# Kernel optimization log

Measured on AMD Instinct MI355X. Metric: run time of the kernel, lower is better.

Reference implementation:

```python
import jax, jax.numpy as jnp
import numpy as np

T, N, E, F_IN, H1, H2, NUM_GRAPHS, K = 8, 10000, 320000, 32, 32, 16, 64, 5


def setup_inputs() -> dict:
    key = jax.random.key(0)
    ks = jax.random.split(key, 16)
    p = lambda k, shape: jax.random.normal(k, shape, jnp.float32) * 0.05
    return {
        "x": jax.random.normal(ks[0], (T, N, F_IN), jnp.float32),
        "edge_index": jax.random.randint(ks[1], (2, E), 0, N),
        "edge_attr": jax.random.uniform(ks[2], (E,), jnp.float32),
        "batch": jnp.sort(jax.random.randint(ks[3], (N,), 0, NUM_GRAPHS)),
        "Wx1": p(ks[4], (4, K, F_IN, H1)),
        "bx1": jnp.zeros((4, H1), jnp.float32),
        "Wh1": p(ks[5], (4, K, H1, H1)),
        "bh1": jnp.zeros((4, H1), jnp.float32),
        "wc1": p(ks[6], (3, H1)),
        "b1": jnp.zeros((4, H1), jnp.float32),
        "Wx2": p(ks[7], (4, K, H1, H2)),
        "bx2": jnp.zeros((4, H2), jnp.float32),
        "Wh2": p(ks[8], (4, K, H2, H2)),
        "bh2": jnp.zeros((4, H2), jnp.float32),
        "wc2": p(ks[9], (3, H2)),
        "b2": jnp.zeros((4, H2), jnp.float32),
        "lin_w": p(ks[10], (H2, 1)),
        "lin_b": jnp.zeros((1,), jnp.float32),
    }


def _forward(x, edge_index, edge_attr, batch,
             Wx1, bx1, Wh1, bh1, wc1, b1,
             Wx2, bx2, Wh2, bh2, wc2, b2, lin_w, lin_b):
    src, dst = edge_index[0], edge_index[1]
    n = x.shape[1]

    # ChebConv sym normalization with lambda_max=2: L_hat = L_sym - I = -D^{-1/2} A D^{-1/2}
    deg = jax.ops.segment_sum(edge_attr, src, num_segments=n)
    deg_safe = jnp.where(deg > 0, deg, 1.0)
    dis = jnp.where(deg > 0, jax.lax.rsqrt(deg_safe), 0.0)
    wnorm = dis[src] * edge_attr * dis[dst]  # [E]

    def Lhat(z):  # z: [N, C] -> L_hat @ z
        return -jax.ops.segment_sum(wnorm[:, None] * z[src], dst, num_segments=n)

    def cheb(z, W, b):  # W: [K, C_in, C_out], b: [C_out]
        out = z @ W[0]
        Tp, Tc = z, Lhat(z)  # T_0, T_1
        out = out + Tc @ W[1]
        for k in range(2, W.shape[0]):
            Tp, Tc = Tc, 2.0 * Lhat(Tc) - Tp
            out = out + Tc @ W[k]
        return out + b

    def cell(X, H, C, Wx, bx, Wh, bh, wc, bg):
        # gate order: 0=i, 1=f, 2=c, 3=o (GConvLSTM with peepholes)
        I = jax.nn.sigmoid(cheb(X, Wx[0], bx[0]) + cheb(H, Wh[0], bh[0]) + wc[0] * C + bg[0])
        Fg = jax.nn.sigmoid(cheb(X, Wx[1], bx[1]) + cheb(H, Wh[1], bh[1]) + wc[1] * C + bg[1])
        Ct = jnp.tanh(cheb(X, Wx[2], bx[2]) + cheb(H, Wh[2], bh[2]) + bg[2])
        Cn = Fg * C + I * Ct
        O = jax.nn.sigmoid(cheb(X, Wx[3], bx[3]) + cheb(H, Wh[3], bh[3]) + wc[2] * Cn + bg[3])
        return O * jnp.tanh(Cn), Cn

    @jax.checkpoint
    def step(carry, xt):
        h1, c1, h2, c2 = carry
        h1, c1 = cell(xt, h1, c1, Wx1, bx1, Wh1, bh1, wc1, b1)
        h2, c2 = cell(h1, h2, c2, Wx2, bx2, Wh2, bh2, wc2, b2)
        return (h1, c1, h2, c2), None

    z32 = jnp.zeros((n, Wh1.shape[-1]), x.dtype)
    z16 = jnp.zeros((n, Wh2.shape[-1]), x.dtype)
    (h1, c1, h2, c2), _ = jax.lax.scan(step, (z32, z32, z16, z16), x)

    # relu/dropout on h2 in the torch code is dead code (its result is unused in eval)
    u = jax.ops.segment_sum(h2, batch, num_segments=NUM_GRAPHS)  # global_add_pool
    return (u @ lin_w + lin_b).reshape(-1)


def reference(x, edge_index, edge_attr, batch,
              Wx1, bx1, Wh1, bh1, wc1, b1,
              Wx2, bx2, Wh2, bh2, wc2, b2, lin_w, lin_b):
    return _forward(x, edge_index, edge_attr, batch,
                    Wx1, bx1, Wh1, bh1, wc1, b1,
                    Wx2, bx2, Wh2, bh2, wc2, b2, lin_w, lin_b)
```

## Files before the change

kernel.cpp:

```cpp
#include <hip/hip_runtime.h>
#include <hip/hip_bf16.h>

#define TT 8
#define NN 10000
#define EE 320000
#define NG 64
#define SZH 384

typedef short v8s __attribute__((ext_vector_type(8)));
typedef _Float16 v8h __attribute__((ext_vector_type(8)));
typedef float v4f __attribute__((ext_vector_type(4)));

__device__ __forceinline__ float sigmf(float x){ return 1.f/(1.f+expf(-x)); }
__device__ __forceinline__ unsigned short f2h(float f){ _Float16 h=(_Float16)f; return __builtin_bit_cast(unsigned short,h); }
__device__ __forceinline__ float h2f(unsigned short s){ return (float)__builtin_bit_cast(_Float16,s); }
__device__ __forceinline__ unsigned pack2h(float x,float y){ return (unsigned)f2h(x) | ((unsigned)f2h(y)<<16); }
__device__ __forceinline__ size_t fragidx(int TK,int row,int c){
  int tile=row>>4, m=row&15, kt=c>>5, cc=c&31;
  return ((size_t)(tile*TK+kt)*64 + (cc>>3)*16 + m)*8 + (cc&7);
}

__device__ __forceinline__ float fetchW1(const float* Wx, const float* Wh, int kk, int col){
  int g=col>>5, j=col&31;
  if(kk<160){ int k=kk>>5, i=kk&31; return Wx[((g*5+k)*32+i)*32+j]; }
  int rr=kk-160; int k=rr>>5, i=rr&31; return Wh[((g*5+k)*32+i)*32+j];
}
__device__ __forceinline__ float fetchW2(const float* Wx, const float* Wh, int kk, int col){
  int g=col>>4, j=col&15;
  if(kk<160){ int k=kk>>5, i=kk&31; return Wx[((g*5+k)*32+i)*16+j]; }
  if(kk<240){ int rr=kk-160; int k=rr>>4, i=rr&15; return Wh[((g*5+k)*16+i)*16+j]; }
  return 0.f;
}

__global__ void k_setup0(const int* __restrict__ src, const int* __restrict__ dst,
                         const float* __restrict__ ea, float* __restrict__ deg, int* __restrict__ cnt,
                         const float* __restrict__ Wx1,const float* __restrict__ bx1,
                         const float* __restrict__ Wh1,const float* __restrict__ bh1,const float* __restrict__ b1,
                         const float* __restrict__ Wx2,const float* __restrict__ bx2,
                         const float* __restrict__ Wh2,const float* __restrict__ bh2,const float* __restrict__ b2g,
                         short* __restrict__ Wpk1, short* __restrict__ Wpk2,
                         float* __restrict__ Bc1,float* __restrict__ Bc2,
                         const float* __restrict__ x, unsigned short* __restrict__ ZH, short* __restrict__ Zb1){
  int idx = blockIdx.x*256+threadIdx.x;
  if(idx<EE){
    atomicAdd(&deg[src[idx]], ea[idx]);
    atomicAdd(&cnt[dst[idx]], 1);
  }
  if(idx < 5120){
    int lane=idx&63, rest=idx>>6;
    int nt=rest&7, kt=rest>>3;
    int col = nt*16 + (lane&15);
    int g = lane>>4;
    #pragma unroll
    for(int j=0;j<8;j++){
      int kk = kt*32 + 8*g + j;
      Wpk1[(size_t)idx*8+j]=(short)f2h(fetchW1(Wx1,Wh1,kk,col));
    }
  } else if(idx < 7168){
    int t=idx-5120;
    int lane=t&63, rest=t>>6;
    int nt=rest&3, kt=rest>>2;
    int col = nt*16 + (lane&15);
    int g = lane>>4;
    #pragma unroll
    for(int j=0;j<8;j++){
      int kk = kt*32 + 8*g + j;
      Wpk2[(size_t)t*8+j]=(short)f2h(fetchW2(Wx2,Wh2,kk,col));
    }
  } else if(idx < 7296){
    int i=idx-7168; int g=i>>5,j=i&31;
    Bc1[i]=bx1[g*32+j]+bh1[g*32+j]+b1[g*32+j];
  } else if(idx < 7360){
    int i=idx-7296; int g=i>>4,j=i&15;
    Bc2[i]=bx2[g*16+j]+bh2[g*16+j]+b2g[g*16+j];
  }
  if(idx<NN*8){
    int n=idx>>3, c4=idx&7;
    float4 v = ((const float4*)x)[idx];
    unsigned p0=pack2h(v.x,v.y), p1=pack2h(v.z,v.w);
    *(unsigned*)&ZH[(size_t)n*SZH + 48 + c4*4]     = p0;
    *(unsigned*)&ZH[(size_t)n*SZH + 48 + c4*4 + 2] = p1;
    size_t fi = fragidx(5, n, c4*4);
    *(unsigned*)&Zb1[fi]   = p0;
    *(unsigned*)&Zb1[fi+2] = p1;
  }
}

__global__ __launch_bounds__(1024) void k_scan2(const int* __restrict__ cnt, int* __restrict__ rowptr,
                                                int* __restrict__ wp, int* __restrict__ lookback){
  __shared__ int wsum[16];
  __shared__ int blocksum_sh;
  __shared__ int prevsum_sh;
  int b=blockIdx.x, tid=threadIdx.x, lane=tid&63, wv=tid>>6;
  int i = b*1024 + tid;
  int v = (i<NN)? cnt[i] : 0;
  int s=v;
  #pragma unroll
  for(int d=1;d<64;d<<=1){ int t=__shfl_up(s,d,64); if(lane>=d) s+=t; }
  if(lane==63) wsum[wv]=s;
  __syncthreads();
  if(wv==0 && lane<16){
    int t=wsum[lane]; int ss=t;
    #pragma unroll
    for(int d=1;d<16;d<<=1){ int u=__shfl_up(ss,d,64); if(lane>=d) ss+=u; }
    wsum[lane]=ss-t;
  }
  __syncthreads();
  int incl = wsum[wv] + s;
  if(tid==1023) blocksum_sh = incl;
  __syncthreads();
  if(tid==0){
    int prev=0;
    if(b>0){
      while(true){ int f=atomicAdd(&lookback[b-1],0); if(f!=0){ prev=f-1; break; } }
    }
    atomicExch(&lookback[b], prev + blocksum_sh + 1);
    prevsum_sh = prev;
    if(b==0) rowptr[0]=0;
  }
  __syncthreads();
  int prev = prevsum_sh;
  if(i<NN){
    rowptr[i+1] = prev + incl;
    wp[i]       = prev + incl - v;
  }
}

__global__ void k_wscatter(const int* __restrict__ src, const int* __restrict__ dst,
                           const float* __restrict__ ea, const float* __restrict__ deg,
                           int* __restrict__ wp, int2* __restrict__ pack){
  int e = blockIdx.x*256+threadIdx.x;
  if(e<EE){
    int s=src[e], d=dst[e];
    float ds_=deg[s], dd=deg[d];
    float is = ds_>0.f ? rsqrtf(ds_) : 0.f;
    float id = dd >0.f ? rsqrtf(dd ) : 0.f;
    float w = is*ea[e]*id;
    int pos = atomicAdd(&wp[d],1);
    pack[pos] = make_int2(s*SZH, __float_as_int(w));
  }
}

template<int MODE>
__global__ __launch_bounds__(512) void k_spmm(const int* __restrict__ rowptr, const int2* __restrict__ pack,
    unsigned short* __restrict__ ZH,
    short* __restrict__ Zb1, short* __restrict__ Zb2, int k){
  int wlocal = __builtin_amdgcn_readfirstlane(threadIdx.x>>6);
  int wid = blockIdx.x*8 + wlocal;
  if(wid>=NN) return;
  int l = threadIdx.x&63;
  int ch; bool act;
  if(MODE==0){ ch=48+2*l; act=(l<16); }
  else if(MODE==1){
    if(l<16) ch=2*l; else if(l<24) ch=32+2*(l-16); else ch=48+2*(l-24);
    act=(l<40);
  } else {
    if(l<16) ch=2*l; else ch=32+2*(l-16);
    act=(l<24);
  }
  if(!act) ch=(MODE==2)?0:48;
  int cin_h = (k-1)*96 + ch;
  int base,width,cloc;
  if(ch<32){ base=0; width=32; cloc=ch; }
  else if(ch<48){ base=160; width=16; cloc=ch-32; }
  else { base=240; width=32; cloc=ch-48; }
  int cout = base + k*width + cloc;
  const unsigned short* __restrict__ Zc = ZH + cin_h;
  int e0=rowptr[wid], e1=rowptr[wid+1];
  float accx=0.f, accy=0.f;
  int e=e0;
  for(; e+16<=e1; e+=16){
    float w[16]; unsigned z[16];
    #pragma unroll
    for(int j=0;j<16;j++){
      int2 p=pack[e+j];
      w[j]=__int_as_float(p.y);
      z[j]=*(const unsigned*)&Zc[(unsigned)p.x];
    }
    #pragma unroll
    for(int j=0;j<16;j++){
      accx = fmaf(h2f((unsigned short)(z[j]&0xffffu)), w[j], accx);
      accy = fmaf(h2f((unsigned short)(z[j]>>16)),     w[j], accy);
    }
  }
  for(; e+4<=e1; e+=4){
    float w[4]; unsigned z[4];
    #pragma unroll
    for(int j=0;j<4;j++){ int2 p=pack[e+j]; w[j]=__int_as_float(p.y); z[j]=*(const unsigned*)&Zc[(unsigned)p.x]; }
    #pragma unroll
    for(int j=0;j<4;j++){
      accx = fmaf(h2f((unsigned short)(z[j]&0xffffu)), w[j], accx);
      accy = fmaf(h2f((unsigned short)(z[j]>>16)),     w[j], accy);
    }
  }
  for(; e<e1; ++e){
    int2 p=pack[e];
    unsigned zz=*(const unsigned*)&Zc[(unsigned)p.x];
    float ww=__int_as_float(p.y);
    accx = fmaf(h2f((unsigned short)(zz&0xffffu)), ww, accx);
    accy = fmaf(h2f((unsigned short)(zz>>16)),     ww, accy);
  }
  if(act){
    float alpha=(k==1)?1.f:2.f;
    float vx = -alpha*accx, vy = -alpha*accy;
    if(k>=2){
      unsigned pp=*(const unsigned*)&ZH[(size_t)wid*SZH+(k-2)*96+ch];
      vx -= h2f((unsigned short)(pp&0xffffu));
      vy -= h2f((unsigned short)(pp>>16));
    }
    unsigned hh = pack2h(vx,vy);
    if(k<=3) *(unsigned*)&ZH[(size_t)wid*SZH + k*96 + ch] = hh;
    if(ch<48) *(unsigned*)&Zb2[fragidx(8,wid,cout)] = hh;
    else      *(unsigned*)&Zb1[fragidx(5,wid,cout-240)] = hh;
  }
}

__device__ __forceinline__ void gemm1_dev(int tile,int lane,
        const short* __restrict__ Zb1, const short* __restrict__ Zb2,
        const v8s* __restrict__ H1T0r, v8s* __restrict__ H1T0w,
        const short* __restrict__ Wpk, const float* __restrict__ Bc, const float* __restrict__ wc1,
        float* __restrict__ c1, unsigned short* __restrict__ ZH,
        short* __restrict__ Zb1w, const float* __restrict__ xn){
  const v8s* A1=(const v8s*)Zb1 + (size_t)tile*320 + lane;
  const v8s* A2=(const v8s*)Zb2 + (size_t)tile*512 + lane;
  v8h afr[10];
  #pragma unroll
  for(int kt=0;kt<5;kt++) afr[kt]=__builtin_bit_cast(v8h, A1[kt*64]);
  afr[5]=__builtin_bit_cast(v8h, H1T0r[(size_t)tile*64+lane]);
  #pragma unroll
  for(int kt=1;kt<5;kt++) afr[5+kt]=__builtin_bit_cast(v8h, A2[kt*64]);
  const v8s* Wp=(const v8s*)Wpk;
  v4f acc[8];
  #pragma unroll
  for(int nt=0;nt<8;nt++) acc[nt]=(v4f){0.f,0.f,0.f,0.f};
  #pragma unroll
  for(int kt=0;kt<10;kt++){
    #pragma unroll
    for(int nt=0;nt<8;nt++){
      v8h b=__builtin_bit_cast(v8h, Wp[(kt*8+nt)*64+lane]);
      acc[nt]=__builtin_amdgcn_mfma_f32_16x16x32_f16(afr[kt],b,acc[nt],0,0,0);
    }
  }
  int row0=tile*16;
  int j0=lane&15;
  int r0=row0+(lane>>4)*4;
  #pragma unroll
  for(int reg=0;reg<4;reg++){
    int row=r0+reg;
    #pragma unroll
    for(int jj=0;jj<2;jj++){
      int j=jj*16+j0;
      float c=c1[row*32+j];
      float I =sigmf(acc[0+jj][reg]+Bc[j]      + wc1[j]*c);
      float Fg=sigmf(acc[2+jj][reg]+Bc[32+j]   + wc1[32+j]*c);
      float Ct=tanhf(acc[4+jj][reg]+Bc[64+j]);
      float Cn=Fg*c + I*Ct;
      float O =sigmf(acc[6+jj][reg]+Bc[96+j]   + wc1[64+j]*Cn);
      float h =O*tanhf(Cn);
      c1[row*32+j]=Cn;
      ZH[(size_t)row*SZH + j]=f2h(h);
      ((unsigned short*)H1T0w)[fragidx(1,row,j)]=f2h(h);
    }
    if(xn){
      float2 xv=*(const float2*)&xn[(size_t)row*32 + 2*j0];
      unsigned pr=pack2h(xv.x,xv.y);
      *(unsigned*)&ZH[(size_t)row*SZH + 48 + 2*j0]=pr;
      *(unsigned*)&Zb1w[fragidx(5,row,2*j0)]=pr;
    }
  }
}

__device__ __forceinline__ void gemm2_dev(int tile,int lane,
        const short* __restrict__ Zb2, const v8s* __restrict__ H1T0r,
        const short* __restrict__ Wpk, const float* __restrict__ Bc, const float* __restrict__ wc2,
        float* __restrict__ c2, unsigned short* __restrict__ ZH,
        short* __restrict__ Zb2w, float* __restrict__ u, const int* __restrict__ batch, int last){
  const v8s* Az=(const v8s*)Zb2 + (size_t)tile*512 + lane;
  v8h afr[8];
  afr[0]=__builtin_bit_cast(v8h, H1T0r[(size_t)tile*64+lane]);
  #pragma unroll
  for(int kt=1;kt<8;kt++) afr[kt]=__builtin_bit_cast(v8h, Az[kt*64]);
  const v8s* Wp=(const v8s*)Wpk;
  v4f acc[4];
  #pragma unroll
  for(int nt=0;nt<4;nt++) acc[nt]=(v4f){0.f,0.f,0.f,0.f};
  #pragma unroll
  for(int kt=0;kt<8;kt++){
    #pragma unroll
    for(int nt=0;nt<4;nt++){
      v8h b=__builtin_bit_cast(v8h, Wp[(kt*4+nt)*64+lane]);
      acc[nt]=__builtin_amdgcn_mfma_f32_16x16x32_f16(afr[kt],b,acc[nt],0,0,0);
    }
  }
  int row0=tile*16;
  int j=lane&15;
  int r0=row0+(lane>>4)*4;
  #pragma unroll
  for(int reg=0;reg<4;reg++){
    int row=r0+reg;
    float c=c2[row*16+j];
    float I =sigmf(acc[0][reg]+Bc[j]    +wc2[j]*c);
    float Fg=sigmf(acc[1][reg]+Bc[16+j] +wc2[16+j]*c);
    float Ct=tanhf(acc[2][reg]+Bc[32+j]);
    float Cn=Fg*c+I*Ct;
    float O =sigmf(acc[3][reg]+Bc[48+j] +wc2[32+j]*Cn);
    float h =O*tanhf(Cn);
    c2[row*16+j]=Cn;
    ZH[(size_t)row*SZH + 32 + j]=f2h(h);
    Zb2w[fragidx(8,row,160+j)]=(short)f2h(h);
    if(last) atomicAdd(&u[batch[row]*16+j], h);
  }
}

__global__ __launch_bounds__(256) void k_g1(const short* Zb1, const short* Zb2,
        const v8s* H1T0r, v8s* H1T0w, const short* Wpk1, const float* Bc1, const float* wc1,
        float* c1, unsigned short* ZH, short* Zb1w, const float* xn){
  int wv=threadIdx.x>>6, lane=threadIdx.x&63;
  int tile=blockIdx.x*4+wv;
  if(tile>=625) return;
  gemm1_dev(tile,lane,Zb1,Zb2,H1T0r,H1T0w,Wpk1,Bc1,wc1,c1,ZH,Zb1w,xn);
}

__global__ __launch_bounds__(256) void k_g2(const short* Zb2, const v8s* H1T0r,
        const short* Wpk2, const float* Bc2, const float* wc2,
        float* c2, unsigned short* ZH, short* Zb2w,
        float* u, const int* batch, int last){
  int wv=threadIdx.x>>6, lane=threadIdx.x&63;
  int tile=blockIdx.x*4+wv;
  if(tile>=625) return;
  gemm2_dev(tile,lane,Zb2,H1T0r,Wpk2,Bc2,wc2,c2,ZH,Zb2w,u,batch,last);
}

__global__ __launch_bounds__(256) void k_g12(const short* Zb1, const short* Zb2,
        const v8s* H1T0r, v8s* H1T0w,
        const short* Wpk1, const float* Bc1, const float* wc1, float* c1,
        const short* Wpk2, const float* Bc2, const float* wc2, float* c2,
        unsigned short* ZH, short* Zb1w, short* Zb2w,
        const float* xn, float* u, const int* batch){
  int wv=threadIdx.x>>6, lane=threadIdx.x&63;
  if(blockIdx.x<157){
    int tile=blockIdx.x*4+wv;
    if(tile>=625) return;
    gemm1_dev(tile,lane,Zb1,Zb2,H1T0r,H1T0w,Wpk1,Bc1,wc1,c1,ZH,Zb1w,xn);
  } else {
    int tile=(blockIdx.x-157)*4+wv;
    if(tile>=625) return;
    gemm2_dev(tile,lane,Zb2,H1T0r,Wpk2,Bc2,wc2,c2,ZH,Zb2w,u,batch,0);
  }
}

__global__ void k_final(const float* __restrict__ u, const float* __restrict__ lw, const float* __restrict__ lb,
                        float* __restrict__ out){
  int g=threadIdx.x;
  if(g<NG){
    float s=lb[0];
    #pragma unroll
    for(int j=0;j<16;j++) s += u[g*16+j]*lw[j];
    out[g]=s;
  }
}

extern "C" void kernel_launch(void* const* d_in, const int* in_sizes, int n_in,
                              void* d_out, int out_size, void* d_ws, size_t ws_size,
                              hipStream_t stream){
  const float* x   = (const float*)d_in[0];
  const int*   ei  = (const int*)d_in[1];
  const float* ea  = (const float*)d_in[2];
  const int*   bat = (const int*)d_in[3];
  const float* Wx1=(const float*)d_in[4];  const float* bx1=(const float*)d_in[5];
  const float* Wh1=(const float*)d_in[6];  const float* bh1=(const float*)d_in[7];
  const float* wc1=(const float*)d_in[8];  const float* b1 =(const float*)d_in[9];
  const float* Wx2=(const float*)d_in[10]; const float* bx2=(const float*)d_in[11];
  const float* Wh2=(const float*)d_in[12]; const float* bh2=(const float*)d_in[13];
  const float* wc2=(const float*)d_in[14]; const float* b2 =(const float*)d_in[15];
  const float* lw =(const float*)d_in[16]; const float* lb =(const float*)d_in[17];
  const int* src = ei; const int* dst = ei+EE;

  float* ws = (float*)d_ws;
  size_t off=0;
  auto alloc=[&](size_t n)->float*{ float* p=ws+off; off+=(n+15)&~(size_t)15; return p; };
  float* deg=alloc(NN);
  float* c1=alloc((size_t)NN*32);
  float* c2=alloc((size_t)NN*16);
  float* u =alloc(NG*16);
  int*   cnt=(int*)alloc(NN);
  int*   lookback=(int*)alloc(16);
  unsigned short* ZH=(unsigned short*)alloc((size_t)NN*SZH/2);
  short* Zb1=(short*)alloc(625*5*64*8/2);
  short* Zb2=(short*)alloc(625*8*64*8/2);
  short* H1T0a=(short*)alloc(625*64*8/2);
  short* H1T0b=(short*)alloc(625*64*8/2);
  size_t zeroEnd=off;
  float* wnormUNUSED=alloc(16); (void)wnormUNUSED;
  int*   rowptr=(int*)alloc(NN+1);
  int*   wp=(int*)alloc(NN);
  int2*  pack=(int2*)alloc((size_t)EE*2);
  short* Wpk1=(short*)alloc(5120*4);
  short* Wpk2=(short*)alloc(2048*4);
  float* Bc1=alloc(128);     float* Bc2=alloc(64);
  (void)ws_size; (void)in_sizes; (void)n_in; (void)out_size;
  v8s* H1T0[2] = { (v8s*)H1T0a, (v8s*)H1T0b };

  hipMemsetAsync(d_ws, 0, zeroEnd*sizeof(float), stream);
  k_setup0  <<<1250,256,0,stream>>>(src,dst,ea,deg,cnt,
      Wx1,bx1,Wh1,bh1,b1,Wx2,bx2,Wh2,bh2,b2,Wpk1,Wpk2,Bc1,Bc2, x,ZH,Zb1);
  k_scan2   <<<10,1024,0,stream>>>(cnt,rowptr,wp,lookback);
  k_wscatter<<<1250,256,0,stream>>>(src,dst,ea,deg,wp,pack);

  for(int k=1;k<5;k++)
    k_spmm<0><<<1250,512,0,stream>>>(rowptr,pack,ZH,Zb1,Zb2,k);

  k_g1<<<157,256,0,stream>>>(Zb1,Zb2,H1T0[1],H1T0[0],Wpk1,Bc1,wc1,c1,ZH,Zb1, x+(size_t)NN*32);

  for(int t=0;t<TT-1;t++){
    for(int k=1;k<5;k++)
      k_spmm<1><<<1250,512,0,stream>>>(rowptr,pack,ZH,Zb1,Zb2,k);
    k_g12<<<314,256,0,stream>>>(Zb1,Zb2,H1T0[t&1],H1T0[(t+1)&1],
        Wpk1,Bc1,wc1,c1, Wpk2,Bc2,wc2,c2, ZH,Zb1,Zb2,
        (t+2<TT)? x+(size_t)(t+2)*NN*32 : nullptr, u,bat);
  }
  for(int k=1;k<5;k++)
    k_spmm<2><<<1250,512,0,stream>>>(rowptr,pack,ZH,Zb1,Zb2,k);
  k_g2<<<157,256,0,stream>>>(Zb2,H1T0[(TT-1)&1],Wpk2,Bc2,wc2,c2,ZH,Zb2,u,bat,1);

  k_final<<<1,64,0,stream>>>(u,lw,lb,(float*)d_out);
}
```

Measured before the change: 573.4 us.

## Split degree atomics, use one-wave GEMM blocks, fuse final linear via ticket

Degree and in-degree atomics are spread over two interleaved copies to reduce contention, and the two copies are summed inside the scan kernel. The GEMM kernels now launch one 64-thread wave per block instead of four waves per block, which spreads the tiles across more CUs. The last GEMM kernel absorbs the final linear layer through a last-block ticket counter, removing one kernel launch. The costs are extra workspace, a threadfence and atomic ticket in the last kernel, and smaller blocks.

```diff
diff --git a/kernel.cpp b/kernel.cpp
--- a/kernel.cpp
+++ b/kernel.cpp
@@ -33,7 +33,7 @@
 }
 
 __global__ void k_setup0(const int* __restrict__ src, const int* __restrict__ dst,
-                         const float* __restrict__ ea, float* __restrict__ deg, int* __restrict__ cnt,
+                         const float* __restrict__ ea, float* __restrict__ deg2, int* __restrict__ cnt2,
                          const float* __restrict__ Wx1,const float* __restrict__ bx1,
                          const float* __restrict__ Wh1,const float* __restrict__ bh1,const float* __restrict__ b1,
                          const float* __restrict__ Wx2,const float* __restrict__ bx2,
@@ -43,8 +43,9 @@
                          const float* __restrict__ x, unsigned short* __restrict__ ZH, short* __restrict__ Zb1){
   int idx = blockIdx.x*256+threadIdx.x;
   if(idx<EE){
-    atomicAdd(&deg[src[idx]], ea[idx]);
-    atomicAdd(&cnt[dst[idx]], 1);
+    int sh = (idx&1)*NN;
+    atomicAdd(&deg2[sh+src[idx]], ea[idx]);
+    atomicAdd(&cnt2[sh+dst[idx]], 1);
   }
   if(idx < 5120){
     int lane=idx&63, rest=idx>>6;
@@ -86,14 +87,16 @@
   }
 }
 
-__global__ __launch_bounds__(1024) void k_scan2(const int* __restrict__ cnt, int* __restrict__ rowptr,
-                                                int* __restrict__ wp, int* __restrict__ lookback){
+__global__ __launch_bounds__(1024) void k_scan2(const int* __restrict__ cnt2, int* __restrict__ rowptr,
+                                                int* __restrict__ wp, int* __restrict__ lookback,
+                                                const float* __restrict__ deg2, float* __restrict__ deg){
   __shared__ int wsum[16];
   __shared__ int blocksum_sh;
   __shared__ int prevsum_sh;
   int b=blockIdx.x, tid=threadIdx.x, lane=tid&63, wv=tid>>6;
   int i = b*1024 + tid;
-  int v = (i<NN)? cnt[i] : 0;
+  int v = (i<NN)? (cnt2[i]+cnt2[NN+i]) : 0;
+  if(i<NN) deg[i] = deg2[i]+deg2[NN+i];
   int s=v;
   #pragma unroll
   for(int d=1;d<64;d<<=1){ int t=__shfl_up(s,d,64); if(lane>=d) s+=t; }
@@ -312,51 +315,39 @@
   }
 }
 
-__global__ __launch_bounds__(256) void k_g1(const short* Zb1, const short* Zb2,
+__global__ __launch_bounds__(64) void k_g1(const short* Zb1, const short* Zb2,
         const v8s* H1T0r, v8s* H1T0w, const short* Wpk1, const float* Bc1, const float* wc1,
         float* c1, unsigned short* ZH, short* Zb1w, const float* xn){
-  int wv=threadIdx.x>>6, lane=threadIdx.x&63;
-  int tile=blockIdx.x*4+wv;
-  if(tile>=625) return;
-  gemm1_dev(tile,lane,Zb1,Zb2,H1T0r,H1T0w,Wpk1,Bc1,wc1,c1,ZH,Zb1w,xn);
-}
-
-__global__ __launch_bounds__(256) void k_g2(const short* Zb2, const v8s* H1T0r,
-        const short* Wpk2, const float* Bc2, const float* wc2,
-        float* c2, unsigned short* ZH, short* Zb2w,
-        float* u, const int* batch, int last){
-  int wv=threadIdx.x>>6, lane=threadIdx.x&63;
-  int tile=blockIdx.x*4+wv;
-  if(tile>=625) return;
-  gemm2_dev(tile,lane,Zb2,H1T0r,Wpk2,Bc2,wc2,c2,ZH,Zb2w,u,batch,last);
-}
-
-__global__ __launch_bounds__(256) void k_g12(const short* Zb1, const short* Zb2,
+  gemm1_dev(blockIdx.x,threadIdx.x,Zb1,Zb2,H1T0r,H1T0w,Wpk1,Bc1,wc1,c1,ZH,Zb1w,xn);
+}
+
+__global__ __launch_bounds__(64) void k_g12(const short* Zb1, const short* Zb2,
         const v8s* H1T0r, v8s* H1T0w,
         const short* Wpk1, const float* Bc1, const float* wc1, float* c1,
         const short* Wpk2, const float* Bc2, const float* wc2, float* c2,
         unsigned short* ZH, short* Zb1w, short* Zb2w,
         const float* xn, float* u, const int* batch){
-  int wv=threadIdx.x>>6, lane=threadIdx.x&63;
-  if(blockIdx.x<157){
-    int tile=blockIdx.x*4+wv;
-    if(tile>=625) return;
-    gemm1_dev(tile,lane,Zb1,Zb2,H1T0r,H1T0w,Wpk1,Bc1,wc1,c1,ZH,Zb1w,xn);
-  } else {
-    int tile=(blockIdx.x-157)*4+wv;
-    if(tile>=625) return;
-    gemm2_dev(tile,lane,Zb2,H1T0r,Wpk2,Bc2,wc2,c2,ZH,Zb2w,u,batch,0);
-  }
-}
-
-__global__ void k_final(const float* __restrict__ u, const float* __restrict__ lw, const float* __restrict__ lb,
-                        float* __restrict__ out){
-  int g=threadIdx.x;
-  if(g<NG){
+  int b=blockIdx.x, lane=threadIdx.x;
+  if(b<625) gemm1_dev(b,lane,Zb1,Zb2,H1T0r,H1T0w,Wpk1,Bc1,wc1,c1,ZH,Zb1w,xn);
+  else      gemm2_dev(b-625,lane,Zb2,H1T0r,Wpk2,Bc2,wc2,c2,ZH,Zb2w,u,batch,0);
+}
+
+__global__ __launch_bounds__(64) void k_g2f(const short* Zb2, const v8s* H1T0r,
+        const short* Wpk2, const float* Bc2, const float* wc2,
+        float* c2, unsigned short* ZH, short* Zb2w,
+        float* u, const int* batch, int* ticket,
+        const float* lw, const float* lb, float* out){
+  int lane=threadIdx.x;
+  gemm2_dev(blockIdx.x,lane,Zb2,H1T0r,Wpk2,Bc2,wc2,c2,ZH,Zb2w,u,batch,1);
+  __threadfence();
+  __shared__ int tk;
+  if(lane==0) tk = atomicAdd(ticket,1);
+  __syncthreads();
+  if(tk==624 && lane<NG){
     float s=lb[0];
     #pragma unroll
-    for(int j=0;j<16;j++) s += u[g*16+j]*lw[j];
-    out[g]=s;
+    for(int j=0;j<16;j++) s += atomicAdd(&u[lane*16+j],0.f)*lw[j];
+    out[lane]=s;
   }
 }
 
@@ -379,19 +370,20 @@
   float* ws = (float*)d_ws;
   size_t off=0;
   auto alloc=[&](size_t n)->float*{ float* p=ws+off; off+=(n+15)&~(size_t)15; return p; };
-  float* deg=alloc(NN);
+  float* deg2=alloc(2*NN);
   float* c1=alloc((size_t)NN*32);
   float* c2=alloc((size_t)NN*16);
   float* u =alloc(NG*16);
-  int*   cnt=(int*)alloc(NN);
+  int*   cnt2=(int*)alloc(2*NN);
   int*   lookback=(int*)alloc(16);
+  int*   ticket=(int*)alloc(16);
   unsigned short* ZH=(unsigned short*)alloc((size_t)NN*SZH/2);
   short* Zb1=(short*)alloc(625*5*64*8/2);
   short* Zb2=(short*)alloc(625*8*64*8/2);
   short* H1T0a=(short*)alloc(625*64*8/2);
   short* H1T0b=(short*)alloc(625*64*8/2);
   size_t zeroEnd=off;
-  float* wnormUNUSED=alloc(16); (void)wnormUNUSED;
+  float* deg=alloc(NN);
   int*   rowptr=(int*)alloc(NN+1);
   int*   wp=(int*)alloc(NN);
   int2*  pack=(int2*)alloc((size_t)EE*2);
@@ -402,26 +394,24 @@
   v8s* H1T0[2] = { (v8s*)H1T0a, (v8s*)H1T0b };
 
   hipMemsetAsync(d_ws, 0, zeroEnd*sizeof(float), stream);
-  k_setup0  <<<1250,256,0,stream>>>(src,dst,ea,deg,cnt,
+  k_setup0  <<<1250,256,0,stream>>>(src,dst,ea,deg2,cnt2,
       Wx1,bx1,Wh1,bh1,b1,Wx2,bx2,Wh2,bh2,b2,Wpk1,Wpk2,Bc1,Bc2, x,ZH,Zb1);
-  k_scan2   <<<10,1024,0,stream>>>(cnt,rowptr,wp,lookback);
+  k_scan2   <<<10,1024,0,stream>>>(cnt2,rowptr,wp,lookback,deg2,deg);
   k_wscatter<<<1250,256,0,stream>>>(src,dst,ea,deg,wp,pack);
 
   for(int k=1;k<5;k++)
     k_spmm<0><<<1250,512,0,stream>>>(rowptr,pack,ZH,Zb1,Zb2,k);
 
-  k_g1<<<157,256,0,stream>>>(Zb1,Zb2,H1T0[1],H1T0[0],Wpk1,Bc1,wc1,c1,ZH,Zb1, x+(size_t)NN*32);
+  k_g1<<<625,64,0,stream>>>(Zb1,Zb2,H1T0[1],H1T0[0],Wpk1,Bc1,wc1,c1,ZH,Zb1, x+(size_t)NN*32);
 
   for(int t=0;t<TT-1;t++){
     for(int k=1;k<5;k++)
       k_spmm<1><<<1250,512,0,stream>>>(rowptr,pack,ZH,Zb1,Zb2,k);
-    k_g12<<<314,256,0,stream>>>(Zb1,Zb2,H1T0[t&1],H1T0[(t+1)&1],
+    k_g12<<<1250,64,0,stream>>>(Zb1,Zb2,H1T0[t&1],H1T0[(t+1)&1],
         Wpk1,Bc1,wc1,c1, Wpk2,Bc2,wc2,c2, ZH,Zb1,Zb2,
         (t+2<TT)? x+(size_t)(t+2)*NN*32 : nullptr, u,bat);
   }
   for(int k=1;k<5;k++)
     k_spmm<2><<<1250,512,0,stream>>>(rowptr,pack,ZH,Zb1,Zb2,k);
-  k_g2<<<157,256,0,stream>>>(Zb2,H1T0[(TT-1)&1],Wpk2,Bc2,wc2,c2,ZH,Zb2,u,bat,1);
-
-  k_final<<<1,64,0,stream>>>(u,lw,lb,(float*)d_out);
-}
+  k_g2f<<<625,64,0,stream>>>(Zb2,H1T0[(TT-1)&1],Wpk2,Bc2,wc2,c2,ZH,Zb2,u,bat,ticket,lw,lb,(float*)d_out);
+}
```

New measurement: 578.4 us. About the same (+0.9%).
